# Optimization experiments

Measured on AMD Instinct MI355X. Metric: run time of the kernel, lower is better.

The kernel has to match this reference:

```python
import jax, jax.numpy as jnp
import numpy as np

D_MODEL = 1024
NHEAD = 16
HEAD_DIM = D_MODEL // NHEAD
SCALE = 1.0 / np.sqrt(HEAD_DIM).astype(np.float32)
B, L = 2, 2048
NEG_INF = -1e30


def setup_inputs() -> dict:
    key = jax.random.key(0)
    ks = jax.random.split(key, 12)
    xav = np.sqrt(6.0 / (D_MODEL + D_MODEL)).astype(np.float32)  # xavier_uniform gain=1
    def lin_w(k):
        return jax.random.uniform(k, (D_MODEL, D_MODEL), jnp.float32, -xav, xav)
    x = jax.random.normal(ks[0], (B, L, D_MODEL), jnp.float32)
    role_mask = jax.random.randint(ks[1], (B, L), 0, 2, jnp.int32)
    # causal attention mask: True = masked (upper triangle above diagonal)
    attn_mask = jnp.triu(jnp.ones((L, L), jnp.bool_), k=1)
    # random key padding: True = padded key
    key_padding_mask = jax.random.randint(ks[2], (B, L), 0, 2, jnp.int32).astype(jnp.bool_)
    return {
        "x": x,
        "role_mask": role_mask,
        "attn_mask": attn_mask,
        "key_padding_mask": key_padding_mask,
        "Wq": lin_w(ks[3]), "bq": jnp.zeros((D_MODEL,), jnp.float32),
        "Wk": lin_w(ks[4]), "bk": jnp.zeros((D_MODEL,), jnp.float32),
        "Wv": lin_w(ks[5]), "bv": jnp.zeros((D_MODEL,), jnp.float32),
        "Wo": lin_w(ks[6]), "bo": jnp.zeros((D_MODEL,), jnp.float32),
        "delta": jnp.asarray(1.0, jnp.float32),
    }


def reference(x, role_mask, attn_mask, key_padding_mask,
              Wq, bq, Wk, bk, Wv, bv, Wo, bo, delta):
    Bb, Ll, Dd = x.shape
    def heads(t):  # [B,L,D] -> [B,H,L,hd]
        return t.reshape(Bb, Ll, NHEAD, HEAD_DIM).transpose(0, 2, 1, 3)
    Q = heads(x @ Wq.T + bq)
    K = heads(x @ Wk.T + bk)
    V = heads(x @ Wv.T + bv)
    scores = jnp.einsum('bhqd,bhkd->bhqk', Q, K) * SCALE  # [B,H,L,L]
    same_role = (role_mask[:, :, None] == role_mask[:, None, :])  # [B,L,L]
    scores = scores + (same_role.astype(scores.dtype) * delta)[:, None, :, :]
    scores = jnp.where(attn_mask[None, None, :, :], -jnp.inf, scores)
    scores = jnp.where(key_padding_mask[:, None, None, :], -jnp.inf, scores)
    attn = jax.nn.softmax(scores, axis=-1)
    attn = jnp.nan_to_num(attn, nan=0.0, posinf=0.0, neginf=0.0)
    out = jnp.einsum('bhqk,bhkd->bhqd', attn, V)
    out = out.transpose(0, 2, 1, 3).reshape(Bb, Ll, Dd)
    return out @ Wo.T + bo
```

## Files before the change

### kernel.cpp

```cpp
#include <hip/hip_runtime.h>
#include <hip/hip_bf16.h>

#define DM 1024
#define NH 16
#define HD 64
#define BB 2
#define LL 2048
#define SCALE 0.125f
#define NEG_BIG -1e30f
#define LOG2E 1.4426950408889634f
#define SC2 (SCALE * LOG2E)
#define FIXM 16.0f

typedef __bf16 bf16;
typedef __bf16 bf16x8 __attribute__((ext_vector_type(8)));
typedef __bf16 bf16x4 __attribute__((ext_vector_type(4)));
typedef float f32x4 __attribute__((ext_vector_type(4)));

static __device__ inline bf16x8 load8(const bf16* p) {
    return *reinterpret_cast<const bf16x8*>(p);
}

static __device__ inline float scrub(float x) {
    union { float f; unsigned u; } c; c.f = x;
    return ((c.u & 0x7F800000u) == 0x7F800000u) ? 0.f : x;
}

typedef __attribute__((address_space(1))) const unsigned char ga_t;
typedef __attribute__((address_space(3))) unsigned char ls_t;
static __device__ inline void gload_lds16(const void* g, void* l) {
    __builtin_amdgcn_global_load_lds((ga_t*)g, (ls_t*)l, 16, 0, 0);
}

__global__ __launch_bounds__(256) void prep_all(
    const float* __restrict__ x,
    const float* __restrict__ Wq, const float* __restrict__ Wk,
    const float* __restrict__ Wv, const float* __restrict__ Wo,
    bf16* __restrict__ xb, bf16* __restrict__ Wqb, bf16* __restrict__ Wkb,
    bf16* __restrict__ Wvb, bf16* __restrict__ Wob,
    const int* __restrict__ role, const void* __restrict__ kpad,
    const float* __restrict__ deltap, float2* __restrict__ biasG)
{
    const int tid = threadIdx.x;
    const int gid = blockIdx.x;
    if (gid < 2048) {
        const float* src; bf16* dst; size_t base;
        if (gid < 1024) { src = x; dst = xb; base = (size_t)gid * 1024; }
        else {
            const int wsel = (gid - 1024) >> 8;
            src = (wsel == 0) ? Wq : (wsel == 1) ? Wk : (wsel == 2) ? Wv : Wo;
            dst = (wsel == 0) ? Wqb : (wsel == 1) ? Wkb : (wsel == 2) ? Wvb : Wob;
            base = (size_t)((gid - 1024) & 255) * 1024;
        }
#pragma unroll
        for (int it = 0; it < 4; it++) {
            const size_t i = base + it * 256 + tid;
            const f32x4 v = ((const f32x4*)src)[i];
            bf16x4 o;
            o[0] = (bf16)v[0]; o[1] = (bf16)v[1]; o[2] = (bf16)v[2]; o[3] = (bf16)v[3];
            ((bf16x4*)dst)[i] = o;
        }
        return;
    }
    const unsigned char* kb = (const unsigned char*)kpad;
    int f3F = 0, fLow = 0, fOff = 0;
    for (int i = (tid & 63); i < BB * LL; i += 64) {
        const unsigned char v = kb[i];
        if (v == 0x3F) f3F = 1;
        if ((i & 3) < 2 && v) fLow = 1;
        if ((i & 3) && v) fOff = 1;
    }
    const int mode = __any(f3F) ? (__any(fLow) ? 3 : 2) : (__any(fOff) ? 1 : 0);
    const float d2 = scrub(deltap[0]) * LOG2E;
    const int idx = (gid - 2048) * 256 + tid;
    const bool pad = (mode == 0) ? (((const int*)kpad)[idx] != 0)
                   : (mode == 1) ? (((const unsigned char*)kpad)[idx] != 0)
                   : (mode == 2) ? (((const float*)kpad)[idx] != 0.f)
                                 : (((const unsigned short*)kpad)[idx] != 0);
    const int r = role[idx];
    const float base = (pad ? NEG_BIG : 0.f) - FIXM;
    float2 o;
    o.x = base + ((r == 0) ? d2 : 0.f);
    o.y = base + ((r == 1) ? d2 : 0.f);
    biasG[idx] = o;
}

__global__ __launch_bounds__(256) void qkv_bf16(
    const bf16* __restrict__ xb,
    const bf16* __restrict__ Wqb, const bf16* __restrict__ Wkb, const bf16* __restrict__ Wvb,
    const float* __restrict__ bq, const float* __restrict__ bk, const float* __restrict__ bv,
    bf16* __restrict__ qw, bf16* __restrict__ kw, bf16* __restrict__ vw)
{
    __shared__ bf16 As[128 * 32];
    __shared__ bf16 Bs[128 * 32];
    const int tid = threadIdx.x;
    const int lane = tid & 63, w = tid >> 6;
    const int wm = w >> 1, wn = w & 1;
    const int ln = lane & 15, quad = lane >> 4;

    const int m0 = blockIdx.x * 128;
    const int sel = blockIdx.y >> 3;
    const int nloc0 = (blockIdx.y & 7) * 128;

    const bf16* Wb = (sel == 0) ? Wqb : ((sel == 1) ? Wkb : Wvb);
    const float* bias = (sel == 0) ? bq : ((sel == 1) ? bk : bv);

    const int rA = lane >> 2;
    const int cA = (lane & 3) * 8;

    f32x4 acc[4][4] = {};
    for (int k0 = 0; k0 < DM; k0 += 32) {
        __syncthreads();
#pragma unroll
        for (int s = 0; s < 2; s++) {
            const int r0 = s * 64 + w * 16;
            gload_lds16(xb + (size_t)(m0 + r0 + rA) * DM + k0 + cA, &As[r0 * 32]);
            gload_lds16(Wb + (size_t)(nloc0 + r0 + rA) * DM + k0 + cA, &Bs[r0 * 32]);
        }
        __syncthreads();
        bf16x8 a[4], b[4];
#pragma unroll
        for (int mi = 0; mi < 4; mi++)
            a[mi] = *(bf16x8*)&As[(wm * 64 + mi * 16 + ln) * 32 + quad * 8];
#pragma unroll
        for (int ni = 0; ni < 4; ni++)
            b[ni] = *(bf16x8*)&Bs[(wn * 64 + ni * 16 + ln) * 32 + quad * 8];
#pragma unroll
        for (int mi = 0; mi < 4; mi++)
#pragma unroll
            for (int ni = 0; ni < 4; ni++)
                acc[mi][ni] = __builtin_amdgcn_mfma_f32_16x16x32_bf16(a[mi], b[ni], acc[mi][ni], 0, 0, 0);
    }

#pragma unroll
    for (int mi = 0; mi < 4; mi++) {
#pragma unroll
        for (int ni = 0; ni < 4; ni++) {
            const int ncol = nloc0 + wn * 64 + ni * 16 + ln;
            const float bv_ = bias[ncol];
            const int hh = ncol >> 6, dd = ncol & 63;
#pragma unroll
            for (int i = 0; i < 4; i++) {
                const int row = m0 + wm * 64 + mi * 16 + quad * 4 + i;
                const int bb = row >> 11, llr = row & (LL - 1);
                const bf16 v = (bf16)scrub(acc[mi][ni][i] + bv_);
                const size_t idx = (((size_t)(bb * NH + hh) * LL) + llr) * HD + dd;
                if (sel == 0)      qw[idx] = v;
                else if (sel == 1) kw[idx] = v;
                else               vw[idx] = v;
            }
        }
    }
}

__global__ __launch_bounds__(256) void vtrans(
    const bf16* __restrict__ vw, bf16* __restrict__ vtw)
{
    __shared__ bf16 T[64 * 72];
    const int tid = threadIdx.x;
    const int bh = blockIdx.x >> 5;
    const int l0 = (blockIdx.x & 31) * 64;
    const size_t base = (size_t)bh * LL * HD;

#pragma unroll
    for (int pass = 0; pass < 2; pass++) {
        const int e = pass * 2048 + tid * 8;
        const int r = e >> 6, c = e & 63;
        *(bf16x8*)&T[r * 72 + c] = load8(vw + base + (size_t)(l0 + r) * HD + c);
    }
    __syncthreads();
#pragma unroll
    for (int pass = 0; pass < 2; pass++) {
        const int e = pass * 2048 + tid * 8;
        const int d = e >> 6, lc = e & 63;
        bf16x8 v;
#pragma unroll
        for (int j = 0; j < 8; j++) v[j] = T[(lc + j) * 72 + d];
        *(bf16x8*)(vtw + base + (size_t)d * LL + l0 + lc) = v;
    }
}

#define PSTR 40
__global__ __launch_bounds__(256) void attn_v6(
    const bf16* __restrict__ qw, const bf16* __restrict__ kw, const bf16* __restrict__ vtw,
    const int* __restrict__ role, const float2* __restrict__ biasG,
    bf16* __restrict__ attn_out)
{
    __shared__ bf16 Ks[2][2][64 * 32];
    __shared__ bf16 Vs[2][2][64 * 32];
    __shared__ bf16 Ps[4][2][2][16 * PSTR];

    const int tid = threadIdx.x;
    const int lane = tid & 63, w = tid >> 6;
    const int col = lane & 15, quad = lane >> 4;
    const int Q = 15 - (blockIdx.x & 15);
    const int bh = blockIdx.x >> 4;
    const int h = bh & (NH - 1), b = bh >> 4;

    const bf16* qbase = qw + (size_t)((b * NH + h) * LL) * HD;
    const bf16* kbase = kw + (size_t)((b * NH + h) * LL) * HD;
    const bf16* vbase = vtw + (size_t)((b * NH + h) * HD) * LL;
    const float2* bias2 = biasG + (size_t)b * LL;
    const int* rrow = role + b * LL;

    const int srow = lane >> 2;
    const int scol = (lane & 3) * 8;
    const bf16* ksrc = kbase + (size_t)(w * 16 + srow) * HD + scol;
    const bf16* vsrc = vbase + (size_t)(w * 16 + srow) * LL + scol;

    int qr[2];
    qr[0] = Q * 128 + w * 16;
    qr[1] = Q * 128 + 64 + w * 16;

    bf16x8 qf[2][2];
    int role_q[2][4];
#pragma unroll
    for (int rg = 0; rg < 2; rg++) {
        qf[rg][0] = load8(qbase + (size_t)(qr[rg] + col) * HD + quad * 8);
        qf[rg][1] = load8(qbase + (size_t)(qr[rg] + col) * HD + 32 + quad * 8);
#pragma unroll
        for (int i = 0; i < 4; i++) role_q[rg][i] = rrow[qr[rg] + quad * 4 + i];
    }

    float lacc[2][4] = {};
    f32x4 o[2][4] = {};

    const int nkt = 2 * Q + 2;

#pragma unroll
    for (int st = 0; st < 2; st++)
        gload_lds16(ksrc + st * 32, &Ks[0][st][w * 512]);
#pragma unroll
    for (int kh = 0; kh < 2; kh++)
        gload_lds16(vsrc + kh * 32, &Vs[0][kh][w * 512]);

    for (int kt = 0; kt < nkt; kt++) {
        const int cur = kt & 1;
        __syncthreads();

        if (kt + 1 < nkt) {
            const int k1 = (kt + 1) * 64;
#pragma unroll
            for (int st = 0; st < 2; st++)
                gload_lds16(ksrc + (size_t)k1 * HD + st * 32, &Ks[cur ^ 1][st][w * 512]);
#pragma unroll
            for (int kh = 0; kh < 2; kh++)
                gload_lds16(vsrc + k1 + kh * 32, &Vs[cur ^ 1][kh][w * 512]);
        }

        const int k0 = kt * 64;
        const bool rg0_on = (kt < nkt - 1);

        float2 bb[4];
#pragma unroll
        for (int ns = 0; ns < 4; ns++) bb[ns] = bias2[k0 + ns * 16 + col];

        f32x4 s[2][4] = {};
#pragma unroll
        for (int st = 0; st < 2; st++) {
#pragma unroll
            for (int ns = 0; ns < 4; ns++) {
                const bf16x8 kf = *(bf16x8*)&Ks[cur][st][(ns * 16 + col) * 32 + quad * 8];
                s[0][ns] = __builtin_amdgcn_mfma_f32_16x16x32_bf16(qf[0][st], kf, s[0][ns], 0, 0, 0);
                s[1][ns] = __builtin_amdgcn_mfma_f32_16x16x32_bf16(qf[1][st], kf, s[1][ns], 0, 0, 0);
            }
        }
#pragma unroll
        for (int rg = 0; rg < 2; rg++) {
            if (rg == 0 && !rg0_on) continue;
            const bool diag = (kt == nkt - 2 + rg);
#pragma unroll
            for (int ns = 0; ns < 4; ns++) {
                const int kk = k0 + ns * 16 + col;
#pragma unroll
                for (int i = 0; i < 4; i++) {
                    float sv = fmaf(s[rg][ns][i], SC2, role_q[rg][i] ? bb[ns].y : bb[ns].x);
                    if (diag && kk > qr[rg] + quad * 4 + i) sv = NEG_BIG;
                    const float p = exp2f(fminf(sv, 14.f));
                    lacc[rg][i] += p;
                    Ps[w][rg][ns >> 1][(quad * 4 + i) * PSTR + (ns & 1) * 16 + col] = (bf16)p;
                }
            }
        }
        bf16x8 pf[2][2];
#pragma unroll
        for (int rg = 0; rg < 2; rg++)
#pragma unroll
            for (int st = 0; st < 2; st++)
                pf[rg][st] = *(bf16x8*)&Ps[w][rg][st][col * PSTR + quad * 8];
#pragma unroll
        for (int ns = 0; ns < 4; ns++) {
#pragma unroll
            for (int kh = 0; kh < 2; kh++) {
                const bf16x8 vf = *(bf16x8*)&Vs[cur][kh][(ns * 16 + col) * 32 + quad * 8];
                if (rg0_on)
                    o[0][ns] = __builtin_amdgcn_mfma_f32_16x16x32_bf16(pf[0][kh], vf, o[0][ns], 0, 0, 0);
                o[1][ns] = __builtin_amdgcn_mfma_f32_16x16x32_bf16(pf[1][kh], vf, o[1][ns], 0, 0, 0);
            }
        }
    }

    bf16* orow = attn_out + (size_t)(b * LL) * DM;
#pragma unroll
    for (int rg = 0; rg < 2; rg++) {
#pragma unroll
        for (int i = 0; i < 4; i++) {
            float l = lacc[rg][i];
#pragma unroll
            for (int off = 8; off > 0; off >>= 1)
                l += __shfl_xor(l, off, 16);
            const float inv = (l > 0.f) ? 1.f / l : 0.f;
            const int qq = qr[rg] + quad * 4 + i;
#pragma unroll
            for (int ns = 0; ns < 4; ns++)
                orow[(size_t)qq * DM + h * HD + ns * 16 + col] = (bf16)scrub(o[rg][ns][i] * inv);
        }
    }
}

__global__ __launch_bounds__(256) void out_bf16(
    const bf16* __restrict__ A, const bf16* __restrict__ Wb,
    const float* __restrict__ bias, float* __restrict__ out)
{
    __shared__ bf16 As[128 * 32];
    __shared__ bf16 Bs[64 * 32];
    const int tid = threadIdx.x;
    const int lane = tid & 63, w = tid >> 6;
    const int ln = lane & 15, quad = lane >> 4;
    const int m0 = blockIdx.x * 128;
    const int n0 = blockIdx.y * 64;

    const int rA = lane >> 2;
    const int cA = (lane & 3) * 8;

    f32x4 acc[2][4] = {};
    for (int k0 = 0; k0 < DM; k0 += 32) {
        __syncthreads();
#pragma unroll
        for (int s = 0; s < 2; s++) {
            const int r0 = s * 64 + w * 16;
            gload_lds16(A + (size_t)(m0 + r0 + rA) * DM + k0 + cA, &As[r0 * 32]);
        }
        gload_lds16(Wb + (size_t)(n0 + w * 16 + rA) * DM + k0 + cA, &Bs[w * 16 * 32]);
        __syncthreads();
        bf16x8 a[2], b[4];
#pragma unroll
        for (int mi = 0; mi < 2; mi++)
            a[mi] = *(bf16x8*)&As[(w * 32 + mi * 16 + ln) * 32 + quad * 8];
#pragma unroll
        for (int ni = 0; ni < 4; ni++)
            b[ni] = *(bf16x8*)&Bs[(ni * 16 + ln) * 32 + quad * 8];
#pragma unroll
        for (int mi = 0; mi < 2; mi++)
#pragma unroll
            for (int ni = 0; ni < 4; ni++)
                acc[mi][ni] = __builtin_amdgcn_mfma_f32_16x16x32_bf16(a[mi], b[ni], acc[mi][ni], 0, 0, 0);
    }
#pragma unroll
    for (int mi = 0; mi < 2; mi++) {
#pragma unroll
        for (int ni = 0; ni < 4; ni++) {
            const int ncol = n0 + ni * 16 + ln;
            const float bv_ = bias[ncol];
#pragma unroll
            for (int i = 0; i < 4; i++) {
                const int row = m0 + w * 32 + mi * 16 + quad * 4 + i;
                out[(size_t)row * DM + ncol] = scrub(acc[mi][ni][i] + bv_);
            }
        }
    }
}

extern "C" void kernel_launch(void* const* d_in, const int* in_sizes, int n_in,
                              void* d_out, int out_size, void* d_ws, size_t ws_size,
                              hipStream_t stream) {
    const float* x    = (const float*)d_in[0];
    const int*   role = (const int*)d_in[1];
    const void*  kpad = d_in[3];
    const float* Wq = (const float*)d_in[4];
    const float* bq = (const float*)d_in[5];
    const float* Wk = (const float*)d_in[6];
    const float* bk = (const float*)d_in[7];
    const float* Wv = (const float*)d_in[8];
    const float* bv = (const float*)d_in[9];
    const float* Wo = (const float*)d_in[10];
    const float* bo = (const float*)d_in[11];
    const float* dl = (const float*)d_in[12];

    char* ws = (char*)d_ws;
    bf16* qw   = (bf16*)(ws);
    bf16* kw   = (bf16*)(ws + (size_t)(8u  << 20));
    bf16* vnat = (bf16*)(ws + (size_t)(16u << 20));
    bf16* aw   = (bf16*)(ws + (size_t)(24u << 20));
    bf16* xb   = (bf16*)(ws + (size_t)(32u << 20));
    bf16* vtw  = xb;
    bf16* Wqb  = (bf16*)(ws + (size_t)(40u << 20));
    bf16* Wkb  = (bf16*)(ws + (size_t)(42u << 20));
    bf16* Wvb  = (bf16*)(ws + (size_t)(44u << 20));
    bf16* Wob  = (bf16*)(ws + (size_t)(46u << 20));
    float2* biasG = (float2*)(ws + (size_t)(48u << 20));
    float* out = (float*)d_out;

    prep_all<<<dim3(2064), dim3(256), 0, stream>>>(
        x, Wq, Wk, Wv, Wo, xb, Wqb, Wkb, Wvb, Wob, role, kpad, dl, biasG);
    qkv_bf16<<<dim3(32, 24), dim3(256), 0, stream>>>(xb, Wqb, Wkb, Wvb, bq, bk, bv, qw, kw, vnat);
    vtrans<<<dim3(BB * NH * (LL / 64)), dim3(256), 0, stream>>>(vnat, vtw);
    attn_v6<<<dim3(BB * NH * (LL / 128)), dim3(256), 0, stream>>>(qw, kw, vtw, role, biasG, aw);
    out_bf16<<<dim3(32, 16), dim3(256), 0, stream>>>(aw, Wob, bo, out);
}
```

Baseline: 260.1 us.

## Split causal attention across KV chunks with a separate combine kernel

Replaces the 128-row query-block attention kernel with a 64-row version that splits the key range into chunks of up to 12 tiles (split-K / flash-decoding style). Long query blocks write unnormalized partial outputs and row sums into scratch pools that reuse the dead V and weight buffers, and a new combine kernel sums the partials and normalizes them. The aim is to balance the causal triangle's uneven work across more blocks, at the cost of an extra launch, scratch-memory traffic and bf16 rounding of the partials. It depends on a fixed max-free softmax (exp2 clamped at 14), so partials can be summed directly without rescaling.

```diff
diff --git a/kernel.cpp b/kernel.cpp
--- a/kernel.cpp
+++ b/kernel.cpp
@@ -11,6 +11,8 @@
 #define LOG2E 1.4426950408889634f
 #define SC2 (SCALE * LOG2E)
 #define FIXM 16.0f
+#define SLOTB 8448
+#define POOL0_SLOTS 960
 
 typedef __bf16 bf16;
 typedef __bf16 bf16x8 __attribute__((ext_vector_type(8)));
@@ -181,21 +183,27 @@
 }
 
 #define PSTR 40
-__global__ __launch_bounds__(256) void attn_v6(
+__global__ __launch_bounds__(256) void attn_v7(
     const bf16* __restrict__ qw, const bf16* __restrict__ kw, const bf16* __restrict__ vtw,
     const int* __restrict__ role, const float2* __restrict__ biasG,
+    char* __restrict__ pool0, char* __restrict__ pool1,
     bf16* __restrict__ attn_out)
 {
+    const int qb = 31 - (blockIdx.x / 3);
+    const int c = blockIdx.x % 3;
+    const int nch = (qb + 12) / 12;
+    if (c >= nch) return;
+
     __shared__ bf16 Ks[2][2][64 * 32];
     __shared__ bf16 Vs[2][2][64 * 32];
-    __shared__ bf16 Ps[4][2][2][16 * PSTR];
+    __shared__ bf16 Ps[4][2][16 * PSTR];
 
     const int tid = threadIdx.x;
     const int lane = tid & 63, w = tid >> 6;
     const int col = lane & 15, quad = lane >> 4;
-    const int Q = 15 - (blockIdx.x & 15);
-    const int bh = blockIdx.x >> 4;
+    const int bh = blockIdx.y;
     const int h = bh & (NH - 1), b = bh >> 4;
+    const int q0 = qb * 64 + w * 16;
 
     const bf16* qbase = qw + (size_t)((b * NH + h) * LL) * HD;
     const bf16* kbase = kw + (size_t)((b * NH + h) * LL) * HD;
@@ -208,37 +216,35 @@
     const bf16* ksrc = kbase + (size_t)(w * 16 + srow) * HD + scol;
     const bf16* vsrc = vbase + (size_t)(w * 16 + srow) * LL + scol;
 
-    int qr[2];
-    qr[0] = Q * 128 + w * 16;
-    qr[1] = Q * 128 + 64 + w * 16;
-
-    bf16x8 qf[2][2];
-    int role_q[2][4];
-#pragma unroll
-    for (int rg = 0; rg < 2; rg++) {
-        qf[rg][0] = load8(qbase + (size_t)(qr[rg] + col) * HD + quad * 8);
-        qf[rg][1] = load8(qbase + (size_t)(qr[rg] + col) * HD + 32 + quad * 8);
-#pragma unroll
-        for (int i = 0; i < 4; i++) role_q[rg][i] = rrow[qr[rg] + quad * 4 + i];
-    }
-
-    float lacc[2][4] = {};
-    f32x4 o[2][4] = {};
-
-    const int nkt = 2 * Q + 2;
-
-#pragma unroll
-    for (int st = 0; st < 2; st++)
-        gload_lds16(ksrc + st * 32, &Ks[0][st][w * 512]);
-#pragma unroll
-    for (int kh = 0; kh < 2; kh++)
-        gload_lds16(vsrc + kh * 32, &Vs[0][kh][w * 512]);
-
-    for (int kt = 0; kt < nkt; kt++) {
-        const int cur = kt & 1;
+    bf16x8 qf[2];
+    qf[0] = load8(qbase + (size_t)(q0 + col) * HD + quad * 8);
+    qf[1] = load8(qbase + (size_t)(q0 + col) * HD + 32 + quad * 8);
+
+    int role_q[4];
+#pragma unroll
+    for (int i = 0; i < 4; i++) role_q[i] = rrow[q0 + quad * 4 + i];
+
+    float lacc[4] = {0.f, 0.f, 0.f, 0.f};
+    f32x4 o[4] = {};
+
+    const int t0 = c * 12;
+    const int t1 = (t0 + 12 < qb + 1) ? t0 + 12 : qb + 1;
+
+    {
+        const int kp = t0 * 64;
+#pragma unroll
+        for (int st = 0; st < 2; st++)
+            gload_lds16(ksrc + (size_t)kp * HD + st * 32, &Ks[0][st][w * 512]);
+#pragma unroll
+        for (int kh = 0; kh < 2; kh++)
+            gload_lds16(vsrc + kp + kh * 32, &Vs[0][kh][w * 512]);
+    }
+
+    for (int kt = t0; kt < t1; kt++) {
+        const int cur = (kt - t0) & 1;
         __syncthreads();
 
-        if (kt + 1 < nkt) {
+        if (kt + 1 < t1) {
             const int k1 = (kt + 1) * 64;
 #pragma unroll
             for (int st = 0; st < 2; st++)
@@ -249,73 +255,130 @@
         }
 
         const int k0 = kt * 64;
-        const bool rg0_on = (kt < nkt - 1);
-
         float2 bb[4];
 #pragma unroll
         for (int ns = 0; ns < 4; ns++) bb[ns] = bias2[k0 + ns * 16 + col];
 
-        f32x4 s[2][4] = {};
+        f32x4 s[4] = {};
 #pragma unroll
         for (int st = 0; st < 2; st++) {
 #pragma unroll
             for (int ns = 0; ns < 4; ns++) {
                 const bf16x8 kf = *(bf16x8*)&Ks[cur][st][(ns * 16 + col) * 32 + quad * 8];
-                s[0][ns] = __builtin_amdgcn_mfma_f32_16x16x32_bf16(qf[0][st], kf, s[0][ns], 0, 0, 0);
-                s[1][ns] = __builtin_amdgcn_mfma_f32_16x16x32_bf16(qf[1][st], kf, s[1][ns], 0, 0, 0);
+                s[ns] = __builtin_amdgcn_mfma_f32_16x16x32_bf16(qf[st], kf, s[ns], 0, 0, 0);
             }
         }
-#pragma unroll
-        for (int rg = 0; rg < 2; rg++) {
-            if (rg == 0 && !rg0_on) continue;
-            const bool diag = (kt == nkt - 2 + rg);
-#pragma unroll
-            for (int ns = 0; ns < 4; ns++) {
-                const int kk = k0 + ns * 16 + col;
-#pragma unroll
-                for (int i = 0; i < 4; i++) {
-                    float sv = fmaf(s[rg][ns][i], SC2, role_q[rg][i] ? bb[ns].y : bb[ns].x);
-                    if (diag && kk > qr[rg] + quad * 4 + i) sv = NEG_BIG;
-                    const float p = exp2f(fminf(sv, 14.f));
-                    lacc[rg][i] += p;
-                    Ps[w][rg][ns >> 1][(quad * 4 + i) * PSTR + (ns & 1) * 16 + col] = (bf16)p;
-                }
+        const bool diag = (kt == qb);
+#pragma unroll
+        for (int ns = 0; ns < 4; ns++) {
+            const int kk = k0 + ns * 16 + col;
+#pragma unroll
+            for (int i = 0; i < 4; i++) {
+                float sv = fmaf(s[ns][i], SC2, role_q[i] ? bb[ns].y : bb[ns].x);
+                if (diag && kk > q0 + quad * 4 + i) sv = NEG_BIG;
+                const float p = exp2f(fminf(sv, 14.f));
+                lacc[i] += p;
+                Ps[w][ns >> 1][(quad * 4 + i) * PSTR + (ns & 1) * 16 + col] = (bf16)p;
             }
         }
-        bf16x8 pf[2][2];
-#pragma unroll
-        for (int rg = 0; rg < 2; rg++)
-#pragma unroll
-            for (int st = 0; st < 2; st++)
-                pf[rg][st] = *(bf16x8*)&Ps[w][rg][st][col * PSTR + quad * 8];
+        bf16x8 pf[2];
+#pragma unroll
+        for (int st = 0; st < 2; st++)
+            pf[st] = *(bf16x8*)&Ps[w][st][col * PSTR + quad * 8];
 #pragma unroll
         for (int ns = 0; ns < 4; ns++) {
 #pragma unroll
             for (int kh = 0; kh < 2; kh++) {
                 const bf16x8 vf = *(bf16x8*)&Vs[cur][kh][(ns * 16 + col) * 32 + quad * 8];
-                if (rg0_on)
-                    o[0][ns] = __builtin_amdgcn_mfma_f32_16x16x32_bf16(pf[0][kh], vf, o[0][ns], 0, 0, 0);
-                o[1][ns] = __builtin_amdgcn_mfma_f32_16x16x32_bf16(pf[1][kh], vf, o[1][ns], 0, 0, 0);
+                o[ns] = __builtin_amdgcn_mfma_f32_16x16x32_bf16(pf[kh], vf, o[ns], 0, 0, 0);
             }
         }
     }
 
-    bf16* orow = attn_out + (size_t)(b * LL) * DM;
-#pragma unroll
-    for (int rg = 0; rg < 2; rg++) {
+    if (nch == 1) {
+        bf16* orow = attn_out + (size_t)(b * LL) * DM;
 #pragma unroll
         for (int i = 0; i < 4; i++) {
-            float l = lacc[rg][i];
+            float l = lacc[i];
 #pragma unroll
             for (int off = 8; off > 0; off >>= 1)
                 l += __shfl_xor(l, off, 16);
             const float inv = (l > 0.f) ? 1.f / l : 0.f;
-            const int qq = qr[rg] + quad * 4 + i;
+            const int qq = q0 + quad * 4 + i;
 #pragma unroll
             for (int ns = 0; ns < 4; ns++)
-                orow[(size_t)qq * DM + h * HD + ns * 16 + col] = (bf16)scrub(o[rg][ns][i] * inv);
-        }
-    }
+                orow[(size_t)qq * DM + h * HD + ns * 16 + col] = (bf16)scrub(o[ns][i] * inv);
+        }
+    } else {
+        const int base = (qb <= 23) ? (qb - 12) * 2 : 24 + (qb - 24) * 3;
+        const int slot = bh * 48 + base + c;
+        char* ptr = (slot < POOL0_SLOTS) ? (pool0 + (size_t)slot * SLOTB)
+                                         : (pool1 + (size_t)(slot - POOL0_SLOTS) * SLOTB);
+        bf16* op = (bf16*)ptr;
+        float* lp = (float*)(ptr + 8192);
+#pragma unroll
+        for (int i = 0; i < 4; i++) {
+            float l = lacc[i];
+#pragma unroll
+            for (int off = 8; off > 0; off >>= 1)
+                l += __shfl_xor(l, off, 16);
+            const int r = w * 16 + quad * 4 + i;
+            if (col == 0) lp[r] = l;
+#pragma unroll
+            for (int ns = 0; ns < 4; ns++)
+                op[r * 64 + ns * 16 + col] = (bf16)scrub(o[ns][i]);
+        }
+    }
+}
+
+__global__ __launch_bounds__(256) void combine(
+    const char* __restrict__ pool0, const char* __restrict__ pool1,
+    bf16* __restrict__ attn_out)
+{
+    const int qb = 12 + blockIdx.x;
+    const int bh = blockIdx.y;
+    const int h = bh & (NH - 1), b = bh >> 4;
+    const int nch = (qb + 12) / 12;
+    const int base = (qb <= 23) ? (qb - 12) * 2 : 24 + (qb - 24) * 3;
+
+    const char* ptr[3];
+    for (int c = 0; c < nch; c++) {
+        const int slot = bh * 48 + base + c;
+        ptr[c] = (slot < POOL0_SLOTS) ? (pool0 + (size_t)slot * SLOTB)
+                                      : (pool1 + (size_t)(slot - POOL0_SLOTS) * SLOTB);
+    }
+
+    __shared__ float linv[64];
+    const int tid = threadIdx.x;
+    if (tid < 64) {
+        float ls = 0.f;
+        for (int c = 0; c < nch; c++) ls += ((const float*)(ptr[c] + 8192))[tid];
+        linv[tid] = (ls > 0.f) ? 1.f / ls : 0.f;
+    }
+    __syncthreads();
+
+    const int r = tid >> 2;
+    const int d0 = (tid & 3) * 16;
+    float acc[16] = {};
+    for (int c = 0; c < nch; c++) {
+        const bf16* op = (const bf16*)ptr[c];
+#pragma unroll
+        for (int half = 0; half < 2; half++) {
+            const bf16x8 v = load8(op + r * 64 + d0 + half * 8);
+#pragma unroll
+            for (int j = 0; j < 8; j++) acc[half * 8 + j] += (float)v[j];
+        }
+    }
+    const float inv = linv[r];
+    bf16x8 outv[2];
+#pragma unroll
+    for (int half = 0; half < 2; half++)
+#pragma unroll
+        for (int j = 0; j < 8; j++)
+            outv[half][j] = (bf16)scrub(acc[half * 8 + j] * inv);
+    bf16* orow = attn_out + ((size_t)(b * LL) + qb * 64 + r) * DM + h * HD + d0;
+    *(bf16x8*)orow = outv[0];
+    *(bf16x8*)(orow + 8) = outv[1];
 }
 
 __global__ __launch_bounds__(256) void out_bf16(
@@ -399,12 +462,15 @@
     bf16* Wvb  = (bf16*)(ws + (size_t)(44u << 20));
     bf16* Wob  = (bf16*)(ws + (size_t)(46u << 20));
     float2* biasG = (float2*)(ws + (size_t)(48u << 20));
+    char* pool0 = (char*)vnat;
+    char* pool1 = (char*)Wqb;
     float* out = (float*)d_out;
 
     prep_all<<<dim3(2064), dim3(256), 0, stream>>>(
         x, Wq, Wk, Wv, Wo, xb, Wqb, Wkb, Wvb, Wob, role, kpad, dl, biasG);
     qkv_bf16<<<dim3(32, 24), dim3(256), 0, stream>>>(xb, Wqb, Wkb, Wvb, bq, bk, bv, qw, kw, vnat);
     vtrans<<<dim3(BB * NH * (LL / 64)), dim3(256), 0, stream>>>(vnat, vtw);
-    attn_v6<<<dim3(BB * NH * (LL / 128)), dim3(256), 0, stream>>>(qw, kw, vtw, role, biasG, aw);
+    attn_v7<<<dim3(96, 32), dim3(256), 0, stream>>>(qw, kw, vtw, role, biasG, pool0, pool1, aw);
+    combine<<<dim3(20, 32), dim3(256), 0, stream>>>(pool0, pool1, aw);
     out_bf16<<<dim3(32, 16), dim3(256), 0, stream>>>(aw, Wob, bo, out);
 }
```

New measurement: 260.5 us. Within noise of the previous version (+0.1%).
